# Kernel optimization log

Hardware: AMD Instinct MI355X
Metric: run time of the kernel (lower is better)

Reference implementation:

```python
import jax, jax.numpy as jnp
import numpy as np

N_NODES = 50000
N_EDGES = 800000
IN_CH = 64
OUT_CH = 128
POWERS = (0, 1, 2)


def setup_inputs() -> dict:
    key = jax.random.key(0)
    k1, k2, k3, k4 = jax.random.split(key, 4)
    x = jax.random.normal(k1, (N_NODES, IN_CH), dtype=jnp.float32)
    edge_index = jax.random.randint(k2, (2, N_EDGES), 0, N_NODES, dtype=jnp.int64)
    fan_in = IN_CH * len(POWERS)
    bound = 1.0 / np.sqrt(fan_in)
    W = jax.random.uniform(k3, (OUT_CH, fan_in), dtype=jnp.float32, minval=-bound, maxval=bound)
    b = jax.random.uniform(k4, (OUT_CH,), dtype=jnp.float32, minval=-bound, maxval=bound)
    return {"x": x, "edge_index": edge_index, "W": W, "b": b}


def _propagate_steps(x, edge_index, max_power):
    # propagated[0] = x; propagated[k] = scatter-add of propagated[k-1][src] into dst
    src, dst = edge_index[0], edge_index[1]
    hops = [x]
    h = x
    for _ in range(max_power):
        h = jax.ops.segment_sum(h[src], dst, num_segments=x.shape[0])
        hops.append(h)
    return hops


def reference(x, edge_index, W, b):
    hops = _propagate_steps(x, edge_index, max(POWERS))
    feats = jnp.concatenate([hops[p] for p in POWERS], axis=-1)  # [N, in*len(powers)]
    return feats @ W.T + b  # [N, out]
```

## Files before the change

### kernel.cpp

```cpp
#include <hip/hip_runtime.h>

#define N_NODES 50000
#define N_EDGES 800000
#define IN_CH   64
#define OUT_CH  128
#define FEAT    192
#define NBK     ((N_NODES + 255) / 256)
#define EPB     4096
#define NPB     ((N_EDGES + EPB - 1) / EPB)
#define N_TILES (N_NODES / 16)
#define CAST_BLOCKS  ((N_NODES * IN_CH / 8 + 255) / 256)
#define WFRAG_BLOCKS ((FEAT * OUT_CH + 255) / 256)

typedef __attribute__((ext_vector_type(8))) short short8;
typedef __attribute__((ext_vector_type(4))) float f32x4;

static __device__ __forceinline__ unsigned short f2bf(float f) {
  unsigned int u = __float_as_uint(f);
  u += 0x7FFFu + ((u >> 16) & 1u);
  return (unsigned short)(u >> 16);
}
static __device__ __forceinline__ float bf2f(unsigned int s) {
  return __uint_as_float(s << 16);
}

__global__ __launch_bounds__(256) void hist_prep_kernel(
    const int* __restrict__ ei, const float* __restrict__ x,
    const float* __restrict__ W, int* __restrict__ hist_t,
    unsigned short* __restrict__ xb, unsigned short* __restrict__ Wf) {
  if (blockIdx.x < NPB) {
    __shared__ int lh[NBK];
    const int b = blockIdx.x;
    for (int i = threadIdx.x; i < NBK; i += 256) lh[i] = 0;
    __syncthreads();
    const int e0 = b * EPB;
    const int e1 = (e0 + EPB < N_EDGES) ? e0 + EPB : N_EDGES;
    for (int e = e0 + threadIdx.x; e < e1; e += 256)
      atomicAdd(&lh[((unsigned)ei[N_EDGES + e]) >> 8], 1);
    __syncthreads();
    for (int k = threadIdx.x; k < NBK; k += 256) hist_t[k * NPB + b] = lh[k];
  } else if (blockIdx.x < NPB + CAST_BLOCKS) {
    const int t = (blockIdx.x - NPB) * 256 + threadIdx.x;
    if (t >= (N_NODES * IN_CH) / 8) return;
    const float4 a = reinterpret_cast<const float4*>(x)[t * 2];
    const float4 c = reinterpret_cast<const float4*>(x)[t * 2 + 1];
    union { unsigned int u[4]; uint4 v; } o;
    o.u[0] = (unsigned)f2bf(a.x) | ((unsigned)f2bf(a.y) << 16);
    o.u[1] = (unsigned)f2bf(a.z) | ((unsigned)f2bf(a.w) << 16);
    o.u[2] = (unsigned)f2bf(c.x) | ((unsigned)f2bf(c.y) << 16);
    o.u[3] = (unsigned)f2bf(c.z) | ((unsigned)f2bf(c.w) << 16);
    reinterpret_cast<uint4*>(xb)[t] = o.v;
  } else {
    const int t = (blockIdx.x - NPB - CAST_BLOCKS) * 256 + threadIdx.x;
    if (t >= FEAT * OUT_CH) return;
    const int j = t & 7;
    const int l = (t >> 3) & 63;
    const int nt = (t >> 9) & 7;
    const int kk = t >> 12;
    const int o = nt * 16 + (l & 15);
    const int k = kk * 32 + (l >> 4) * 8 + j;
    Wf[t] = f2bf(W[o * FEAT + k]);
  }
}

__global__ __launch_bounds__(256) void part_scan_kernel(
    const int* __restrict__ hist_t, int* __restrict__ offs_t,
    int* __restrict__ total) {
  __shared__ int s[256];
  const int k = blockIdx.x;
  const int t = threadIdx.x;
  const int v = (t < NPB) ? hist_t[k * NPB + t] : 0;
  s[t] = v;
  __syncthreads();
  for (int off = 1; off < 256; off <<= 1) {
    const int u = (t >= off) ? s[t - off] : 0;
    __syncthreads();
    s[t] += u;
    __syncthreads();
  }
  if (t < NPB) offs_t[k * NPB + t] = s[t] - v;
  if (t == 255) total[k] = s[255];
}

__global__ __launch_bounds__(256) void part_fill_kernel(
    const int* __restrict__ ei, const int* __restrict__ total,
    const int* __restrict__ offs_t, unsigned* __restrict__ pairs) {
  __shared__ int s[256];
  __shared__ int cur[NBK];
  const int b = blockIdx.x;
  const int t = threadIdx.x;
  const int v = (t < NBK) ? total[t] : 0;
  s[t] = v;
  __syncthreads();
  for (int off = 1; off < 256; off <<= 1) {
    const int u = (t >= off) ? s[t - off] : 0;
    __syncthreads();
    s[t] += u;
    __syncthreads();
  }
  if (t < NBK) cur[t] = (s[t] - v) + offs_t[t * NPB + b];
  __syncthreads();

  const int e0 = b * EPB;
  const int e1 = (e0 + EPB < N_EDGES) ? e0 + EPB : N_EDGES;
  for (int e = e0 + t; e < e1; e += 256) {
    const unsigned sv = (unsigned)ei[e];
    const unsigned d = (unsigned)ei[N_EDGES + e];
    const int pos = atomicAdd(&cur[d >> 8], 1);
    pairs[pos] = (sv << 8) | (d & 255u);
  }
}

__global__ __launch_bounds__(256) void bucket_csr_kernel(
    const unsigned* __restrict__ pairs, const int* __restrict__ total,
    int* __restrict__ rowptr, int* __restrict__ srcs) {
  __shared__ int s[256];
  __shared__ int bofs[NBK];
  __shared__ int cnt[256];
  __shared__ int sc[256];
  const int tid = threadIdx.x;
  {
    const int v = (tid < NBK) ? total[tid] : 0;
    s[tid] = v;
    __syncthreads();
    for (int off = 1; off < 256; off <<= 1) {
      const int u = (tid >= off) ? s[tid - off] : 0;
      __syncthreads();
      s[tid] += u;
      __syncthreads();
    }
    if (tid < NBK) bofs[tid] = s[tid] - v;
  }
  __syncthreads();

  const int k = blockIdx.x;
  const int base = bofs[k];
  const int limit = base + total[k];

  cnt[tid] = 0;
  __syncthreads();
  for (int i = base + tid; i < limit; i += 256)
    atomicAdd(&cnt[pairs[i] & 255u], 1);
  __syncthreads();

  const int v = cnt[tid];
  sc[tid] = v;
  __syncthreads();
  for (int off = 1; off < 256; off <<= 1) {
    const int u = (tid >= off) ? sc[tid - off] : 0;
    __syncthreads();
    sc[tid] += u;
    __syncthreads();
  }
  const int ex = base + sc[tid] - v;

  const int node = k * 256 + tid;
  if (node < N_NODES) rowptr[node] = ex;
  if (k == 0 && tid == 0) rowptr[N_NODES] = N_EDGES;

  cnt[tid] = ex;
  __syncthreads();
  for (int i = base + tid; i < limit; i += 256) {
    const unsigned p = pairs[i];
    const int pos = atomicAdd(&cnt[p & 255u], 1);
    srcs[pos] = (int)(p >> 8);
  }
}

__global__ __launch_bounds__(256) void gather_kernel(
    const unsigned short* __restrict__ hin, const int* __restrict__ rowptr,
    const int* __restrict__ srcs, unsigned short* __restrict__ hout) {
  const int gid = blockIdx.x * blockDim.x + threadIdx.x;
  const int node = gid >> 6;
  if (node >= N_NODES) return;
  const int lane = threadIdx.x & 63;
  const int g = lane >> 3;
  const int s = lane & 7;

  const int beg = rowptr[node];
  const int end = rowptr[node + 1];

  float acc[8];
#pragma unroll
  for (int j = 0; j < 8; ++j) acc[j] = 0.0f;

  for (int i = beg + g; i < end; i += 8) {
    const int src = srcs[i];
    const uint4 v = *reinterpret_cast<const uint4*>(
        hin + (size_t)src * IN_CH + s * 8);
    acc[0] += bf2f(v.x & 0xffffu); acc[1] += bf2f(v.x >> 16);
    acc[2] += bf2f(v.y & 0xffffu); acc[3] += bf2f(v.y >> 16);
    acc[4] += bf2f(v.z & 0xffffu); acc[5] += bf2f(v.z >> 16);
    acc[6] += bf2f(v.w & 0xffffu); acc[7] += bf2f(v.w >> 16);
  }

#pragma unroll
  for (int j = 0; j < 8; ++j) {
    acc[j] += __shfl_xor(acc[j], 8);
    acc[j] += __shfl_xor(acc[j], 16);
    acc[j] += __shfl_xor(acc[j], 32);
  }

  if (g == 0) {
    union { unsigned u[4]; uint4 v; } o;
    o.u[0] = (unsigned)f2bf(acc[0]) | ((unsigned)f2bf(acc[1]) << 16);
    o.u[1] = (unsigned)f2bf(acc[2]) | ((unsigned)f2bf(acc[3]) << 16);
    o.u[2] = (unsigned)f2bf(acc[4]) | ((unsigned)f2bf(acc[5]) << 16);
    o.u[3] = (unsigned)f2bf(acc[6]) | ((unsigned)f2bf(acc[7]) << 16);
    *reinterpret_cast<uint4*>(hout + (size_t)node * IN_CH + s * 8) = o.v;
  }
}

__global__ __launch_bounds__(256) void gemm_kernel(
    const unsigned short* __restrict__ xb,
    const unsigned short* __restrict__ h1b,
    const unsigned short* __restrict__ h2b,
    const unsigned short* __restrict__ Wf, const float* __restrict__ b,
    float* __restrict__ out) {
  const int wave = (blockIdx.x * 256 + threadIdx.x) >> 6;
  if (wave >= N_TILES) return;
  const int lane = threadIdx.x & 63;
  const int node0 = wave * 16;
  const int mrow = lane & 15;
  const int kg = lane >> 4;

  f32x4 acc[8];
#pragma unroll
  for (int nt = 0; nt < 8; ++nt) acc[nt] = (f32x4){0.f, 0.f, 0.f, 0.f};

  const unsigned short* const srcarr[3] = {xb, h1b, h2b};
#pragma unroll
  for (int kk = 0; kk < 6; ++kk) {
    const unsigned short* a = srcarr[kk >> 1];
    const short8 af = *reinterpret_cast<const short8*>(
        a + (size_t)(node0 + mrow) * IN_CH + (kk & 1) * 32 + kg * 8);
#pragma unroll
    for (int nt = 0; nt < 8; ++nt) {
      const short8 bf = *reinterpret_cast<const short8*>(
          Wf + ((size_t)(kk * 8 + nt) * 64 + lane) * 8);
      acc[nt] = __builtin_amdgcn_mfma_f32_16x16x32_bf16(af, bf, acc[nt], 0, 0, 0);
    }
  }

#pragma unroll
  for (int nt = 0; nt < 8; ++nt) {
    const int oc = nt * 16 + mrow;
    const float bias = b[oc];
#pragma unroll
    for (int r = 0; r < 4; ++r) {
      out[(size_t)(node0 + kg * 4 + r) * OUT_CH + oc] = acc[nt][r] + bias;
    }
  }
}

extern "C" void kernel_launch(void* const* d_in, const int* in_sizes, int n_in,
                              void* d_out, int out_size, void* d_ws,
                              size_t ws_size, hipStream_t stream) {
  const float* x = (const float*)d_in[0];
  const int* ei = (const int*)d_in[1];
  const float* W = (const float*)d_in[2];
  const float* b = (const float*)d_in[3];
  float* out = (float*)d_out;

  char* p = (char*)d_ws;
  auto take = [&](size_t bytes) {
    char* r = p;
    p += (bytes + 255) & ~(size_t)255;
    return r;
  };
  unsigned short* xb  = (unsigned short*)take((size_t)N_NODES * IN_CH * 2);
  unsigned short* h1b = (unsigned short*)take((size_t)N_NODES * IN_CH * 2);
  unsigned short* h2b = (unsigned short*)take((size_t)N_NODES * IN_CH * 2);
  unsigned short* Wf  = (unsigned short*)take((size_t)FEAT * OUT_CH * 2);
  int* total  = (int*)take((size_t)NBK * 4);
  int* rowptr = (int*)take((size_t)(N_NODES + 1) * 4);
  unsigned* pairs = (unsigned*)take((size_t)N_EDGES * 4);
  int* srcs   = (int*)take((size_t)N_EDGES * 4);
  int* hist_t = (int*)take((size_t)NBK * NPB * 4);
  int* offs_t = (int*)take((size_t)NBK * NPB * 4);

  hist_prep_kernel<<<NPB + CAST_BLOCKS + WFRAG_BLOCKS, 256, 0, stream>>>(
      ei, x, W, hist_t, xb, Wf);
  part_scan_kernel<<<NBK, 256, 0, stream>>>(hist_t, offs_t, total);
  part_fill_kernel<<<NPB, 256, 0, stream>>>(ei, total, offs_t, pairs);
  bucket_csr_kernel<<<NBK, 256, 0, stream>>>(pairs, total, rowptr, srcs);

  const int gblocks = (N_NODES * 64 + 255) / 256;
  gather_kernel<<<gblocks, 256, 0, stream>>>(xb, rowptr, srcs, h1b);
  gather_kernel<<<gblocks, 256, 0, stream>>>(h1b, rowptr, srcs, h2b);

  const int gemmblocks = (N_TILES + 3) / 4;
  gemm_kernel<<<gemmblocks, 256, 0, stream>>>(xb, h1b, h2b, Wf, b, out);
}
```

Measured before the change: 163.5 us.

## Fuse all stages into one persistent cooperative kernel with grid syncs

Replaces the seven separate launches (histogram/cast, scan, fill, CSR build, two gathers, GEMM) with a single cooperative kernel of 512 persistent blocks. Each stage loops over its tasks and stages are separated by grid.sync(). This is meant to remove per-launch overhead and inter-kernel gaps. The cost is grid-wide barriers and lower parallelism, since there are fewer resident blocks to hide gather latency. The multi-kernel path is kept as a fallback if the cooperative launch fails.

```diff
diff --git a/kernel.cpp b/kernel.cpp
--- a/kernel.cpp
+++ b/kernel.cpp
@@ -1,4 +1,7 @@
 #include <hip/hip_runtime.h>
+#include <hip/hip_cooperative_groups.h>
+
+namespace cg = cooperative_groups;
 
 #define N_NODES 50000
 #define N_EDGES 800000
@@ -9,8 +12,11 @@
 #define EPB     4096
 #define NPB     ((N_EDGES + EPB - 1) / EPB)
 #define N_TILES (N_NODES / 16)
-#define CAST_BLOCKS  ((N_NODES * IN_CH / 8 + 255) / 256)
-#define WFRAG_BLOCKS ((FEAT * OUT_CH + 255) / 256)
+#define CAST_TASKS  ((N_NODES * IN_CH / 8 + 255) / 256)
+#define WFRAG_TASKS ((FEAT * OUT_CH + 255) / 256)
+#define GATHER_TASKS ((N_NODES * 64) / 256)
+#define GEMM_TASKS  ((N_TILES + 3) / 4)
+#define GRID    512
 
 typedef __attribute__((ext_vector_type(8))) short short8;
 typedef __attribute__((ext_vector_type(4))) float f32x4;
@@ -24,101 +30,91 @@
   return __uint_as_float(s << 16);
 }
 
-__global__ __launch_bounds__(256) void hist_prep_kernel(
-    const int* __restrict__ ei, const float* __restrict__ x,
-    const float* __restrict__ W, int* __restrict__ hist_t,
-    unsigned short* __restrict__ xb, unsigned short* __restrict__ Wf) {
-  if (blockIdx.x < NPB) {
-    __shared__ int lh[NBK];
-    const int b = blockIdx.x;
-    for (int i = threadIdx.x; i < NBK; i += 256) lh[i] = 0;
-    __syncthreads();
-    const int e0 = b * EPB;
-    const int e1 = (e0 + EPB < N_EDGES) ? e0 + EPB : N_EDGES;
-    for (int e = e0 + threadIdx.x; e < e1; e += 256)
-      atomicAdd(&lh[((unsigned)ei[N_EDGES + e]) >> 8], 1);
-    __syncthreads();
-    for (int k = threadIdx.x; k < NBK; k += 256) hist_t[k * NPB + b] = lh[k];
-  } else if (blockIdx.x < NPB + CAST_BLOCKS) {
-    const int t = (blockIdx.x - NPB) * 256 + threadIdx.x;
-    if (t >= (N_NODES * IN_CH) / 8) return;
-    const float4 a = reinterpret_cast<const float4*>(x)[t * 2];
-    const float4 c = reinterpret_cast<const float4*>(x)[t * 2 + 1];
-    union { unsigned int u[4]; uint4 v; } o;
-    o.u[0] = (unsigned)f2bf(a.x) | ((unsigned)f2bf(a.y) << 16);
-    o.u[1] = (unsigned)f2bf(a.z) | ((unsigned)f2bf(a.w) << 16);
-    o.u[2] = (unsigned)f2bf(c.x) | ((unsigned)f2bf(c.y) << 16);
-    o.u[3] = (unsigned)f2bf(c.z) | ((unsigned)f2bf(c.w) << 16);
-    reinterpret_cast<uint4*>(xb)[t] = o.v;
-  } else {
-    const int t = (blockIdx.x - NPB - CAST_BLOCKS) * 256 + threadIdx.x;
-    if (t >= FEAT * OUT_CH) return;
-    const int j = t & 7;
-    const int l = (t >> 3) & 63;
-    const int nt = (t >> 9) & 7;
-    const int kk = t >> 12;
-    const int o = nt * 16 + (l & 15);
-    const int k = kk * 32 + (l >> 4) * 8 + j;
-    Wf[t] = f2bf(W[o * FEAT + k]);
-  }
-}
-
-__global__ __launch_bounds__(256) void part_scan_kernel(
+
+static __device__ __forceinline__ void dev_hist(int b, int tid, int* lh,
+    const int* __restrict__ ei, int* __restrict__ hist_t) {
+  for (int i = tid; i < NBK; i += 256) lh[i] = 0;
+  __syncthreads();
+  const int e0 = b * EPB;
+  const int e1 = (e0 + EPB < N_EDGES) ? e0 + EPB : N_EDGES;
+  for (int e = e0 + tid; e < e1; e += 256)
+    atomicAdd(&lh[((unsigned)ei[N_EDGES + e]) >> 8], 1);
+  __syncthreads();
+  for (int k = tid; k < NBK; k += 256) hist_t[k * NPB + b] = lh[k];
+  __syncthreads();
+}
+
+static __device__ __forceinline__ void dev_cast(int i,
+    const float* __restrict__ x, unsigned short* __restrict__ xb) {
+  if (i >= (N_NODES * IN_CH) / 8) return;
+  const float4 a = reinterpret_cast<const float4*>(x)[i * 2];
+  const float4 c = reinterpret_cast<const float4*>(x)[i * 2 + 1];
+  union { unsigned u[4]; uint4 v; } o;
+  o.u[0] = (unsigned)f2bf(a.x) | ((unsigned)f2bf(a.y) << 16);
+  o.u[1] = (unsigned)f2bf(a.z) | ((unsigned)f2bf(a.w) << 16);
+  o.u[2] = (unsigned)f2bf(c.x) | ((unsigned)f2bf(c.y) << 16);
+  o.u[3] = (unsigned)f2bf(c.z) | ((unsigned)f2bf(c.w) << 16);
+  reinterpret_cast<uint4*>(xb)[i] = o.v;
+}
+
+static __device__ __forceinline__ void dev_wfrag(int i,
+    const float* __restrict__ W, unsigned short* __restrict__ Wf) {
+  if (i >= FEAT * OUT_CH) return;
+  const int j = i & 7;
+  const int l = (i >> 3) & 63;
+  const int nt = (i >> 9) & 7;
+  const int kk = i >> 12;
+  const int o = nt * 16 + (l & 15);
+  const int k = kk * 32 + (l >> 4) * 8 + j;
+  Wf[i] = f2bf(W[o * FEAT + k]);
+}
+
+static __device__ __forceinline__ void dev_scan(int k, int tid, int* s,
     const int* __restrict__ hist_t, int* __restrict__ offs_t,
     int* __restrict__ total) {
-  __shared__ int s[256];
-  const int k = blockIdx.x;
-  const int t = threadIdx.x;
-  const int v = (t < NPB) ? hist_t[k * NPB + t] : 0;
-  s[t] = v;
+  const int v = (tid < NPB) ? hist_t[k * NPB + tid] : 0;
+  s[tid] = v;
   __syncthreads();
   for (int off = 1; off < 256; off <<= 1) {
-    const int u = (t >= off) ? s[t - off] : 0;
-    __syncthreads();
-    s[t] += u;
-    __syncthreads();
-  }
-  if (t < NPB) offs_t[k * NPB + t] = s[t] - v;
-  if (t == 255) total[k] = s[255];
-}
-
-__global__ __launch_bounds__(256) void part_fill_kernel(
-    const int* __restrict__ ei, const int* __restrict__ total,
+    const int u = (tid >= off) ? s[tid - off] : 0;
+    __syncthreads();
+    s[tid] += u;
+    __syncthreads();
+  }
+  if (tid < NPB) offs_t[k * NPB + tid] = s[tid] - v;
+  if (tid == 255) total[k] = s[255];
+  __syncthreads();
+}
+
+static __device__ __forceinline__ void dev_fill(int b, int tid, int* s,
+    int* cur, const int* __restrict__ ei, const int* __restrict__ total,
     const int* __restrict__ offs_t, unsigned* __restrict__ pairs) {
-  __shared__ int s[256];
-  __shared__ int cur[NBK];
-  const int b = blockIdx.x;
-  const int t = threadIdx.x;
-  const int v = (t < NBK) ? total[t] : 0;
-  s[t] = v;
+  const int v = (tid < NBK) ? total[tid] : 0;
+  s[tid] = v;
   __syncthreads();
   for (int off = 1; off < 256; off <<= 1) {
-    const int u = (t >= off) ? s[t - off] : 0;
-    __syncthreads();
-    s[t] += u;
-    __syncthreads();
-  }
-  if (t < NBK) cur[t] = (s[t] - v) + offs_t[t * NPB + b];
-  __syncthreads();
-
+    const int u = (tid >= off) ? s[tid - off] : 0;
+    __syncthreads();
+    s[tid] += u;
+    __syncthreads();
+  }
+  if (tid < NBK) cur[tid] = (s[tid] - v) + offs_t[tid * NPB + b];
+  __syncthreads();
   const int e0 = b * EPB;
   const int e1 = (e0 + EPB < N_EDGES) ? e0 + EPB : N_EDGES;
-  for (int e = e0 + t; e < e1; e += 256) {
+  for (int e = e0 + tid; e < e1; e += 256) {
     const unsigned sv = (unsigned)ei[e];
     const unsigned d = (unsigned)ei[N_EDGES + e];
     const int pos = atomicAdd(&cur[d >> 8], 1);
     pairs[pos] = (sv << 8) | (d & 255u);
   }
-}
-
-__global__ __launch_bounds__(256) void bucket_csr_kernel(
-    const unsigned* __restrict__ pairs, const int* __restrict__ total,
-    int* __restrict__ rowptr, int* __restrict__ srcs) {
-  __shared__ int s[256];
-  __shared__ int bofs[NBK];
-  __shared__ int cnt[256];
-  __shared__ int sc[256];
-  const int tid = threadIdx.x;
+  __syncthreads();
+}
+
+static __device__ __forceinline__ void dev_csr(int k, int tid, int* s,
+    int* bofs, int* cnt, int* sc, const unsigned* __restrict__ pairs,
+    const int* __restrict__ total, int* __restrict__ rowptr,
+    int* __restrict__ srcs) {
   {
     const int v = (tid < NBK) ? total[tid] : 0;
     s[tid] = v;
@@ -133,7 +129,6 @@
   }
   __syncthreads();
 
-  const int k = blockIdx.x;
   const int base = bofs[k];
   const int limit = base + total[k];
 
@@ -165,17 +160,16 @@
     const int pos = atomicAdd(&cnt[p & 255u], 1);
     srcs[pos] = (int)(p >> 8);
   }
-}
-
-__global__ __launch_bounds__(256) void gather_kernel(
+  __syncthreads();
+}
+
+static __device__ __forceinline__ void dev_gather(int task, int tid,
     const unsigned short* __restrict__ hin, const int* __restrict__ rowptr,
     const int* __restrict__ srcs, unsigned short* __restrict__ hout) {
-  const int gid = blockIdx.x * blockDim.x + threadIdx.x;
-  const int node = gid >> 6;
-  if (node >= N_NODES) return;
-  const int lane = threadIdx.x & 63;
+  const int node = task * 4 + (tid >> 6);
+  const int lane = tid & 63;
   const int g = lane >> 3;
-  const int s = lane & 7;
+  const int sl = lane & 7;
 
   const int beg = rowptr[node];
   const int end = rowptr[node + 1];
@@ -187,7 +181,7 @@
   for (int i = beg + g; i < end; i += 8) {
     const int src = srcs[i];
     const uint4 v = *reinterpret_cast<const uint4*>(
-        hin + (size_t)src * IN_CH + s * 8);
+        hin + (size_t)src * IN_CH + sl * 8);
     acc[0] += bf2f(v.x & 0xffffu); acc[1] += bf2f(v.x >> 16);
     acc[2] += bf2f(v.y & 0xffffu); acc[3] += bf2f(v.y >> 16);
     acc[4] += bf2f(v.z & 0xffffu); acc[5] += bf2f(v.z >> 16);
@@ -207,19 +201,19 @@
     o.u[1] = (unsigned)f2bf(acc[2]) | ((unsigned)f2bf(acc[3]) << 16);
     o.u[2] = (unsigned)f2bf(acc[4]) | ((unsigned)f2bf(acc[5]) << 16);
     o.u[3] = (unsigned)f2bf(acc[6]) | ((unsigned)f2bf(acc[7]) << 16);
-    *reinterpret_cast<uint4*>(hout + (size_t)node * IN_CH + s * 8) = o.v;
-  }
-}
-
-__global__ __launch_bounds__(256) void gemm_kernel(
+    *reinterpret_cast<uint4*>(hout + (size_t)node * IN_CH + sl * 8) = o.v;
+  }
+}
+
+static __device__ __forceinline__ void dev_gemm(int task, int tid,
     const unsigned short* __restrict__ xb,
     const unsigned short* __restrict__ h1b,
     const unsigned short* __restrict__ h2b,
-    const unsigned short* __restrict__ Wf, const float* __restrict__ b,
+    const unsigned short* __restrict__ Wf, const float* __restrict__ bvec,
     float* __restrict__ out) {
-  const int wave = (blockIdx.x * 256 + threadIdx.x) >> 6;
+  const int wave = task * 4 + (tid >> 6);
   if (wave >= N_TILES) return;
-  const int lane = threadIdx.x & 63;
+  const int lane = tid & 63;
   const int node0 = wave * 16;
   const int mrow = lane & 15;
   const int kg = lane >> 4;
@@ -238,19 +232,114 @@
     for (int nt = 0; nt < 8; ++nt) {
       const short8 bf = *reinterpret_cast<const short8*>(
           Wf + ((size_t)(kk * 8 + nt) * 64 + lane) * 8);
-      acc[nt] = __builtin_amdgcn_mfma_f32_16x16x32_bf16(af, bf, acc[nt], 0, 0, 0);
+      acc[nt] =
+          __builtin_amdgcn_mfma_f32_16x16x32_bf16(af, bf, acc[nt], 0, 0, 0);
     }
   }
 
 #pragma unroll
   for (int nt = 0; nt < 8; ++nt) {
     const int oc = nt * 16 + mrow;
-    const float bias = b[oc];
+    const float bias = bvec[oc];
 #pragma unroll
     for (int r = 0; r < 4; ++r) {
       out[(size_t)(node0 + kg * 4 + r) * OUT_CH + oc] = acc[nt][r] + bias;
     }
   }
+}
+
+__global__ __launch_bounds__(256, 2) void fused_kernel(
+    const int* __restrict__ ei, const float* __restrict__ x,
+    const float* __restrict__ W, const float* __restrict__ bvec,
+    float* __restrict__ out, int* __restrict__ hist_t,
+    int* __restrict__ offs_t, int* __restrict__ total,
+    int* __restrict__ rowptr, unsigned* __restrict__ pairs,
+    int* __restrict__ srcs, unsigned short* __restrict__ xb,
+    unsigned short* __restrict__ h1b, unsigned short* __restrict__ h2b,
+    unsigned short* __restrict__ Wf) {
+  cg::grid_group grid = cg::this_grid();
+  __shared__ int smem[1024];
+  const int bid = blockIdx.x;
+  const int tid = threadIdx.x;
+
+  for (int t = bid; t < NPB + CAST_TASKS + WFRAG_TASKS; t += GRID) {
+    if (t < NPB) dev_hist(t, tid, smem, ei, hist_t);
+    else if (t < NPB + CAST_TASKS) dev_cast((t - NPB) * 256 + tid, x, xb);
+    else dev_wfrag((t - NPB - CAST_TASKS) * 256 + tid, W, Wf);
+  }
+  grid.sync();
+  for (int k = bid; k < NBK; k += GRID)
+    dev_scan(k, tid, smem, hist_t, offs_t, total);
+  grid.sync();
+  for (int b2 = bid; b2 < NPB; b2 += GRID)
+    dev_fill(b2, tid, smem, smem + 256, ei, total, offs_t, pairs);
+  grid.sync();
+  for (int k = bid; k < NBK; k += GRID)
+    dev_csr(k, tid, smem, smem + 256, smem + 452, smem + 708, pairs, total,
+            rowptr, srcs);
+  grid.sync();
+  for (int t = bid; t < GATHER_TASKS; t += GRID)
+    dev_gather(t, tid, xb, rowptr, srcs, h1b);
+  grid.sync();
+  for (int t = bid; t < GATHER_TASKS; t += GRID)
+    dev_gather(t, tid, h1b, rowptr, srcs, h2b);
+  grid.sync();
+  for (int t = bid; t < GEMM_TASKS; t += GRID)
+    dev_gemm(t, tid, xb, h1b, h2b, Wf, bvec, out);
+}
+
+__global__ __launch_bounds__(256) void k_hist_prep(
+    const int* __restrict__ ei, const float* __restrict__ x,
+    const float* __restrict__ W, int* __restrict__ hist_t,
+    unsigned short* __restrict__ xb, unsigned short* __restrict__ Wf) {
+  __shared__ int lh[NBK];
+  const int t = blockIdx.x;
+  if (t < NPB) dev_hist(t, threadIdx.x, lh, ei, hist_t);
+  else if (t < NPB + CAST_TASKS) dev_cast((t - NPB) * 256 + threadIdx.x, x, xb);
+  else dev_wfrag((t - NPB - CAST_TASKS) * 256 + threadIdx.x, W, Wf);
+}
+
+__global__ __launch_bounds__(256) void k_scan(const int* __restrict__ hist_t,
+                                              int* __restrict__ offs_t,
+                                              int* __restrict__ total) {
+  __shared__ int s[256];
+  dev_scan(blockIdx.x, threadIdx.x, s, hist_t, offs_t, total);
+}
+
+__global__ __launch_bounds__(256) void k_fill(const int* __restrict__ ei,
+                                              const int* __restrict__ total,
+                                              const int* __restrict__ offs_t,
+                                              unsigned* __restrict__ pairs) {
+  __shared__ int s[256];
+  __shared__ int cur[NBK];
+  dev_fill(blockIdx.x, threadIdx.x, s, cur, ei, total, offs_t, pairs);
+}
+
+__global__ __launch_bounds__(256) void k_csr(const unsigned* __restrict__ pairs,
+                                             const int* __restrict__ total,
+                                             int* __restrict__ rowptr,
+                                             int* __restrict__ srcs) {
+  __shared__ int s[256];
+  __shared__ int bofs[NBK];
+  __shared__ int cnt[256];
+  __shared__ int sc[256];
+  dev_csr(blockIdx.x, threadIdx.x, s, bofs, cnt, sc, pairs, total, rowptr,
+          srcs);
+}
+
+__global__ __launch_bounds__(256) void k_gather(
+    const unsigned short* __restrict__ hin, const int* __restrict__ rowptr,
+    const int* __restrict__ srcs, unsigned short* __restrict__ hout) {
+  dev_gather(blockIdx.x, threadIdx.x, hin, rowptr, srcs, hout);
+}
+
+__global__ __launch_bounds__(256) void k_gemm(
+    const unsigned short* __restrict__ xb,
+    const unsigned short* __restrict__ h1b,
+    const unsigned short* __restrict__ h2b,
+    const unsigned short* __restrict__ Wf, const float* __restrict__ bvec,
+    float* __restrict__ out) {
+  dev_gemm(blockIdx.x, threadIdx.x, xb, h1b, h2b, Wf, bvec, out);
 }
 
 extern "C" void kernel_launch(void* const* d_in, const int* in_sizes, int n_in,
@@ -279,16 +368,22 @@
   int* hist_t = (int*)take((size_t)NBK * NPB * 4);
   int* offs_t = (int*)take((size_t)NBK * NPB * 4);
 
-  hist_prep_kernel<<<NPB + CAST_BLOCKS + WFRAG_BLOCKS, 256, 0, stream>>>(
-      ei, x, W, hist_t, xb, Wf);
-  part_scan_kernel<<<NBK, 256, 0, stream>>>(hist_t, offs_t, total);
-  part_fill_kernel<<<NPB, 256, 0, stream>>>(ei, total, offs_t, pairs);
-  bucket_csr_kernel<<<NBK, 256, 0, stream>>>(pairs, total, rowptr, srcs);
-
-  const int gblocks = (N_NODES * 64 + 255) / 256;
-  gather_kernel<<<gblocks, 256, 0, stream>>>(xb, rowptr, srcs, h1b);
-  gather_kernel<<<gblocks, 256, 0, stream>>>(h1b, rowptr, srcs, h2b);
-
-  const int gemmblocks = (N_TILES + 3) / 4;
-  gemm_kernel<<<gemmblocks, 256, 0, stream>>>(xb, h1b, h2b, Wf, b, out);
-}
+  void* args[] = {(void*)&ei,     (void*)&x,      (void*)&W,
+                  (void*)&b,      (void*)&out,    (void*)&hist_t,
+                  (void*)&offs_t, (void*)&total,  (void*)&rowptr,
+                  (void*)&pairs,  (void*)&srcs,   (void*)&xb,
+                  (void*)&h1b,    (void*)&h2b,    (void*)&Wf};
+  hipError_t cerr = hipLaunchCooperativeKernel(
+      (const void*)fused_kernel, dim3(GRID), dim3(256), args, 0, stream);
+  if (cerr != hipSuccess) {
+    (void)hipGetLastError();
+    k_hist_prep<<<NPB + CAST_TASKS + WFRAG_TASKS, 256, 0, stream>>>(
+        ei, x, W, hist_t, xb, Wf);
+    k_scan<<<NBK, 256, 0, stream>>>(hist_t, offs_t, total);
+    k_fill<<<NPB, 256, 0, stream>>>(ei, total, offs_t, pairs);
+    k_csr<<<NBK, 256, 0, stream>>>(pairs, total, rowptr, srcs);
+    k_gather<<<GATHER_TASKS, 256, 0, stream>>>(xb, rowptr, srcs, h1b);
+    k_gather<<<GATHER_TASKS, 256, 0, stream>>>(h1b, rowptr, srcs, h2b);
+    k_gemm<<<GEMM_TASKS, 256, 0, stream>>>(xb, h1b, h2b, Wf, b, out);
+  }
+}
```

New measurement: 568.1 us. 248% more time.
